# Optimization experiments

Measured on AMD Instinct MI355X. Metric: run time of the kernel, lower is better.

## Reference

```python
import jax, jax.numpy as jnp
import numpy as np

N_NODES = 50000
N_EDGES = 800000
NFEAT, NHID, NCLASS = 512, 128, 16


def _with_self_loops(edge_idx, n):
    loop = jnp.arange(n, dtype=edge_idx.dtype)
    src = jnp.concatenate([edge_idx[0], loop])  # [E+N]
    dst = jnp.concatenate([edge_idx[1], loop])
    return src, dst


def gcn_conv(x, src, dst, W, b, n):
    # GCNConv with add aggregation, self-loops, symmetric normalization.
    h = x @ W  # [N, out]
    ones = jnp.ones(src.shape[0], dtype=h.dtype)
    deg = jax.ops.segment_sum(ones, dst, num_segments=n)  # in-degree incl. self-loops
    dinv = jnp.where(deg > 0, jax.lax.rsqrt(deg), 0.0)
    norm = dinv[src] * dinv[dst]  # [E+N]
    msg = h[src] * norm[:, None]  # gather + scale
    out = jax.ops.segment_sum(msg, dst, num_segments=n)  # scatter-add
    return out + b


def setup_inputs() -> dict:
    key = jax.random.key(0)
    ks = jax.random.split(key, 8)
    x = jax.random.normal(ks[0], (N_NODES, NFEAT), dtype=jnp.float32)
    edge_idx = jax.random.randint(ks[1], (2, N_EDGES), 0, N_NODES, dtype=jnp.int64)
    s1 = 1.0 / np.sqrt(NFEAT)
    s2 = 1.0 / np.sqrt(NHID)
    W1 = jax.random.uniform(ks[2], (NFEAT, NHID), jnp.float32, -s1, s1)
    b1 = jnp.zeros((NHID,), jnp.float32)
    W2 = jax.random.uniform(ks[3], (NHID, NHID), jnp.float32, -s2, s2)
    b2 = jnp.zeros((NHID,), jnp.float32)
    Wc = jax.random.uniform(ks[4], (NHID, NCLASS), jnp.float32, -s2, s2)
    bc = jax.random.uniform(ks[5], (NCLASS,), jnp.float32, -s2, s2)
    return {"x": x, "edge_idx": edge_idx, "W1": W1, "b1": b1, "W2": W2, "b2": b2, "Wc": Wc, "bc": bc}


def reference(x, edge_idx, W1, b1, W2, b2, Wc, bc):
    n = x.shape[0]
    src, dst = _with_self_loops(edge_idx, n)
    h = gcn_conv(x, src, dst, W1, b1, n)
    h = jax.nn.relu(h)  # dropout is identity in eval mode
    h = gcn_conv(h, src, dst, W2, b2, n)
    h = jax.nn.relu(h)
    logits = h @ Wc + bc
    return jax.nn.log_softmax(logits, axis=1)
```

## Files before the change

kernel.cpp:

```cpp
#include <hip/hip_runtime.h>
#include <math.h>

#define NFEAT 512
#define NHID  128
#define NCLASS 16
#define SCAN_BS 512
#define AGG_BLOCKS 1024
#define NSTREAMS 16384

typedef __attribute__((ext_vector_type(8))) short short8;
typedef __attribute__((ext_vector_type(4))) float f32x4;

static __device__ __forceinline__ ushort f2b(float f) {
    union { float f; uint u; } v; v.f = f;
    uint r = v.u + 0x7FFFu + ((v.u >> 16) & 1u);
    return (ushort)(r >> 16);
}
static __device__ __forceinline__ float b2f_lo(uint bits) {
    union { uint u; float f; } v; v.u = bits << 16; return v.f;
}
static __device__ __forceinline__ float b2f_hi(uint bits) {
    union { uint u; float f; } v; v.u = bits & 0xffff0000u; return v.f;
}


__global__ void k_init_tcast(const float* __restrict__ W1, const float* __restrict__ W2,
                             ushort* __restrict__ W1T, ushort* __restrict__ W2T,
                             int* __restrict__ deg, int n) {
    int idx = blockIdx.x * 256 + threadIdx.x;
    if (idx < n) deg[idx] = 1;
    if (idx < NFEAT * 128) {
        int k = idx >> 7, c = idx & 127;
        W1T[(size_t)c * NFEAT + k] = f2b(W1[idx]);
    } else {
        int j = idx - NFEAT * 128;
        if (j < NHID * 128) {
            int k = j >> 7, c = j & 127;
            W2T[(size_t)c * NHID + k] = f2b(W2[j]);
        }
    }
}

__global__ void k_count(const int* __restrict__ dst, int e, int* __restrict__ deg,
                        int* __restrict__ ticket) {
    int i = blockIdx.x * blockDim.x + threadIdx.x;
    if (i < e) ticket[i] = atomicAdd(&deg[dst[i]], 1);
}

__global__ void k_scan1(const int* __restrict__ deg, float* __restrict__ dinv,
                        int* __restrict__ offs, int* __restrict__ bsum, int n) {
    __shared__ int s[SCAN_BS];
    int t = threadIdx.x;
    int i = blockIdx.x * SCAN_BS + t;
    int d = (i < n) ? deg[i] : 0;
    if (i < n) dinv[i] = rsqrtf((float)d);
    s[t] = d;
    for (int off = 1; off < SCAN_BS; off <<= 1) {
        __syncthreads();
        int x = (t >= off) ? s[t - off] : 0;
        __syncthreads();
        s[t] += x;
    }
    __syncthreads();
    if (i < n) offs[i] = s[t] - d;
    if (t == SCAN_BS - 1) bsum[blockIdx.x] = s[t];
}

__global__ void k_fill_edges(const int* __restrict__ src, const int* __restrict__ dst, int e,
                             const int* __restrict__ offs, const int* __restrict__ bsum,
                             const int* __restrict__ ticket, uint* __restrict__ colp32,
                             int* __restrict__ rankgs, int n, int S, int nbch) {
    __shared__ int incl[128];
    int tid = threadIdx.x;
    if (tid < 64) {
        int carry = 0;
        for (int base = 0; base < nbch; base += 64) {
            int j = base + tid;
            int v = (j < nbch) ? bsum[j] : 0;
            for (int off = 1; off < 64; off <<= 1) {
                int x = __shfl_up(v, off);
                if (tid >= off) v += x;
            }
            if (j < nbch) incl[j] = carry + v;
            carry += __shfl(v, 63);
        }
    }
    __syncthreads();

    auto absoff = [&](int v) -> int {
        if (v >= n) return S;
        int c = v >> 9;
        return offs[v] + (c ? incl[c - 1] : 0);
    };

    int i = blockIdx.x * blockDim.x + tid;
    if (i < e) {
        colp32[absoff(dst[i]) + ticket[i] - 1] = (uint)src[i];
    }
    if (i < n) {
        colp32[absoff(i + 1) - 1] = (uint)i | ((uint)(i + 1) << 16);
    }
    if (i < NSTREAMS) {
        int len = (S + NSTREAMS - 1) / NSTREAMS;
        int target = i * len;
        int lo = 0, hi = n;
        while (lo < hi) {
            int mid = (lo + hi) >> 1;
            if (absoff(mid) < target) lo = mid + 1; else hi = mid;
        }
        rankgs[i] = absoff(lo);
        if (i == 0) rankgs[NSTREAMS] = S;
    }
    if (i == 0) {
#pragma unroll
        for (int k = 0; k < 8; k++) colp32[S + k] = 0;
    }
}


template<int A_F32>
__global__ __launch_bounds__(256) void k_gemm(const void* __restrict__ Aptr,
                                              const ushort* __restrict__ WT,
                                              const float* __restrict__ rowscale,
                                              ushort* __restrict__ Hs, int M, int K) {
    __shared__ ushort As[64][40];
    __shared__ ushort Bs[128][40];

    const int tid = threadIdx.x;
    const int wc = tid >> 6, lane = tid & 63;
    const int lr = lane & 15, lk = (lane >> 4) * 8;
    const int rowbase = blockIdx.x * 64;

    f32x4 acc[4][2];
#pragma unroll
    for (int i = 0; i < 4; i++)
#pragma unroll
        for (int j = 0; j < 2; j++) acc[i][j] = (f32x4)0.f;

    const int sr = tid >> 2;
    const int sh = (tid & 3) * 8;

    for (int k0 = 0; k0 < K; k0 += 32) {
        {
            int gr = rowbase + sr;
            ushort tmp[8];
            if (A_F32) {
                const float* A = (const float*)Aptr;
                if (gr < M) {
                    const float* p = A + (size_t)gr * K + k0 + sh;
#pragma unroll
                    for (int q = 0; q < 2; q++) {
                        float4 v = *(const float4*)(p + q * 4);
                        tmp[q * 4 + 0] = f2b(v.x); tmp[q * 4 + 1] = f2b(v.y);
                        tmp[q * 4 + 2] = f2b(v.z); tmp[q * 4 + 3] = f2b(v.w);
                    }
                } else {
#pragma unroll
                    for (int q = 0; q < 8; q++) tmp[q] = 0;
                }
            } else {
                const ushort* A = (const ushort*)Aptr;
                if (gr < M) {
                    *(short8*)&tmp[0] = *(const short8*)(A + (size_t)gr * K + k0 + sh);
                } else {
#pragma unroll
                    for (int q = 0; q < 8; q++) tmp[q] = 0;
                }
            }
            *(short8*)&As[sr][sh] = *(short8*)&tmp[0];
        }
        {
#pragma unroll
            for (int t = 0; t < 2; t++) {
                int c = tid + t * 256;
                int row = c >> 2, q = c & 3;
                short8 v = *(const short8*)(WT + (size_t)row * K + k0 + q * 8);
                *(short8*)&Bs[row][q * 8] = v;
            }
        }
        __syncthreads();

        short8 af[4], bfv[2];
#pragma unroll
        for (int i = 0; i < 4; i++) af[i] = *(const short8*)&As[i * 16 + lr][lk];
#pragma unroll
        for (int j = 0; j < 2; j++) bfv[j] = *(const short8*)&Bs[wc * 32 + j * 16 + lr][lk];
#pragma unroll
        for (int i = 0; i < 4; i++)
#pragma unroll
            for (int j = 0; j < 2; j++)
                acc[i][j] = __builtin_amdgcn_mfma_f32_16x16x32_bf16(af[i], bfv[j], acc[i][j], 0, 0, 0);
        __syncthreads();
    }

#pragma unroll
    for (int i = 0; i < 4; i++) {
#pragma unroll
        for (int r = 0; r < 4; r++) {
            int row = rowbase + i * 16 + (lane >> 4) * 4 + r;
            if (row < M) {
                float sc = rowscale[row];
#pragma unroll
                for (int j = 0; j < 2; j++) {
                    int f = j * 16 + lr;
                    Hs[((size_t)wc * M + row) * 32 + f] = f2b(acc[i][j][r] * sc);
                }
            }
        }
    }
}


__global__ __launch_bounds__(256) void k_aggs(const ushort* __restrict__ hs,
                                              const uint* __restrict__ colp32,
                                              const int* __restrict__ rankgs,
                                              const float* __restrict__ dinv,
                                              const float* __restrict__ bias,
                                              ushort* __restrict__ outp, int n) {
    const int b = blockIdx.x;
    const int s = b & 3;
    const int wid = threadIdx.x >> 6, lane = threadIdx.x & 63;
    const int st16 = lane >> 2, q = lane & 3;
    const int stream = (((b >> 2) << 2) + wid) * 16 + st16;
    int g = rankgs[stream];
    int se = rankgs[stream + 1];
    bool alive = g < se;
    if (!alive) g = 0;

    const ushort* hsl = hs + (size_t)s * n * 32;
    const float4 bv0 = *(const float4*)(bias + s * 32 + q * 8);
    const float4 bv1 = *(const float4*)(bias + s * 32 + q * 8 + 4);

    const uint* cp = colp32 + g;
    uint cw0 = cp[0], cw1 = cp[1], cw2 = cp[2], cw3 = cp[3], cw4 = cp[4];
    uint4 pk0 = *(const uint4*)(hsl + (size_t)(cw0 & 0xffffu) * 32 + q * 8);
    uint4 pk1 = *(const uint4*)(hsl + (size_t)(cw1 & 0xffffu) * 32 + q * 8);
    uint4 pk2 = *(const uint4*)(hsl + (size_t)(cw2 & 0xffffu) * 32 + q * 8);
    uint4 pk3 = *(const uint4*)(hsl + (size_t)(cw3 & 0xffffu) * 32 + q * 8);
    float fdv0 = (cw0 >> 16) ? dinv[(cw0 >> 16) - 1] : 0.f;
    float fdv1 = (cw1 >> 16) ? dinv[(cw1 >> 16) - 1] : 0.f;
    float fdv2 = (cw2 >> 16) ? dinv[(cw2 >> 16) - 1] : 0.f;
    float fdv3 = (cw3 >> 16) ? dinv[(cw3 >> 16) - 1] : 0.f;
    float a0 = 0.f, a1 = 0.f, a2 = 0.f, a3 = 0.f;
    float a4 = 0.f, a5 = 0.f, a6 = 0.f, a7 = 0.f;

    while (__any(alive)) {
        if (alive) {
            uint cw5 = cp[5];
            uint4 pk4 = *(const uint4*)(hsl + (size_t)(cw4 & 0xffffu) * 32 + q * 8);
            float fdv4 = (cw4 >> 16) ? dinv[(cw4 >> 16) - 1] : 0.f;

            a0 += b2f_lo(pk0.x); a1 += b2f_hi(pk0.x);
            a2 += b2f_lo(pk0.y); a3 += b2f_hi(pk0.y);
            a4 += b2f_lo(pk0.z); a5 += b2f_hi(pk0.z);
            a6 += b2f_lo(pk0.w); a7 += b2f_hi(pk0.w);

            if (cw0 >> 16) {
                int v = (int)(cw0 >> 16) - 1;
                float r0 = fmaxf(fmaf(a0, fdv0, bv0.x), 0.f);
                float r1 = fmaxf(fmaf(a1, fdv0, bv0.y), 0.f);
                float r2 = fmaxf(fmaf(a2, fdv0, bv0.z), 0.f);
                float r3 = fmaxf(fmaf(a3, fdv0, bv0.w), 0.f);
                float r4 = fmaxf(fmaf(a4, fdv0, bv1.x), 0.f);
                float r5 = fmaxf(fmaf(a5, fdv0, bv1.y), 0.f);
                float r6 = fmaxf(fmaf(a6, fdv0, bv1.z), 0.f);
                float r7 = fmaxf(fmaf(a7, fdv0, bv1.w), 0.f);
                uint4 u;
                u.x = (uint)f2b(r0) | ((uint)f2b(r1) << 16);
                u.y = (uint)f2b(r2) | ((uint)f2b(r3) << 16);
                u.z = (uint)f2b(r4) | ((uint)f2b(r5) << 16);
                u.w = (uint)f2b(r6) | ((uint)f2b(r7) << 16);
                *(uint4*)(outp + (size_t)v * 128 + s * 32 + q * 8) = u;
                a0 = a1 = a2 = a3 = a4 = a5 = a6 = a7 = 0.f;
                if (g + 1 >= se) alive = false;
            }
            g++; cp++;
            cw0 = cw1; cw1 = cw2; cw2 = cw3; cw3 = cw4; cw4 = cw5;
            pk0 = pk1; pk1 = pk2; pk2 = pk3; pk3 = pk4;
            fdv0 = fdv1; fdv1 = fdv2; fdv2 = fdv3; fdv3 = fdv4;
        }
    }
}


__global__ __launch_bounds__(256) void k_classify(const ushort* __restrict__ h,
                                                  const float* __restrict__ Wc,
                                                  const float* __restrict__ bc,
                                                  float* __restrict__ out, int n) {
    __shared__ float Ws[128 * 16];
    int tid = threadIdx.x;
#pragma unroll
    for (int t = 0; t < 8; t++) Ws[tid + 256 * t] = Wc[tid + 256 * t];
    __syncthreads();

    int wid = tid >> 6, lane = tid & 63;
    int v = blockIdx.x * 4 + wid;
    if (v >= n) return;

    int j = lane & 15, c = lane >> 4;
    const ushort* hv = h + (size_t)v * 128 + c * 32;
    float acc = 0.f;
#pragma unroll
    for (int t = 0; t < 16; t++) {
        uint pk = *(const uint*)(hv + t * 2);
        acc = fmaf(b2f_lo(pk), Ws[(c * 32 + t * 2 + 0) * 16 + j], acc);
        acc = fmaf(b2f_hi(pk), Ws[(c * 32 + t * 2 + 1) * 16 + j], acc);
    }
    acc += __shfl_xor(acc, 16);
    acc += __shfl_xor(acc, 32);
    acc += bc[j];

    float m = acc;
#pragma unroll
    for (int o = 8; o >= 1; o >>= 1) m = fmaxf(m, __shfl_xor(m, o));
    float sum = expf(acc - m);
#pragma unroll
    for (int o = 8; o >= 1; o >>= 1) sum += __shfl_xor(sum, o);
    if (lane < 16) out[(size_t)v * 16 + j] = acc - m - logf(sum);
}


extern "C" void kernel_launch(void* const* d_in, const int* in_sizes, int n_in,
                              void* d_out, int out_size, void* d_ws, size_t ws_size,
                              hipStream_t stream) {
    const float* x  = (const float*)d_in[0];
    const int* eidx = (const int*)d_in[1];
    const float* W1 = (const float*)d_in[2];
    const float* b1 = (const float*)d_in[3];
    const float* W2 = (const float*)d_in[4];
    const float* b2 = (const float*)d_in[5];
    const float* Wc = (const float*)d_in[6];
    const float* bc = (const float*)d_in[7];
    float* out = (float*)d_out;

    const int N = in_sizes[0] / NFEAT;
    const int E = in_sizes[1] / 2;
    const int S = E + N;
    const int* src = eidx;
    const int* dst = eidx + E;

    char* p = (char*)d_ws;
    auto alloc = [&](size_t bytes) { char* r = p; p += (bytes + 255) & ~(size_t)255; return r; };
    int*    deg    = (int*)   alloc((size_t)N * 4);
    float*  dinv   = (float*) alloc((size_t)N * 4);
    int*    eoffs  = (int*)   alloc((size_t)(N + 1) * 4);
    int*    ticket = (int*)   alloc((size_t)E * 4);
    uint*   colp32 = (uint*)  alloc(((size_t)S + 16) * 4);
    int*    rankgs = (int*)   alloc((size_t)(NSTREAMS + 1) * 4);
    int*    bsum   = (int*)   alloc((size_t)256 * 4);
    ushort* W1T    = (ushort*)alloc((size_t)128 * NFEAT * 2);
    ushort* W2T    = (ushort*)alloc((size_t)128 * NHID * 2);
    ushort* hs     = (ushort*)alloc((size_t)N * NHID * 2);
    ushort* g1     = (ushort*)alloc((size_t)N * NHID * 2);
    ushort* g2     = (ushort*)alloc((size_t)N * NHID * 2);

    const int nb = (N + SCAN_BS - 1) / SCAN_BS;

    k_init_tcast<<<((NFEAT + NHID) * 128 + 255) / 256, 256, 0, stream>>>(W1, W2, W1T, W2T, deg, N);
    k_count<<<(E + 255) / 256, 256, 0, stream>>>(dst, E, deg, ticket);
    k_scan1<<<nb, SCAN_BS, 0, stream>>>(deg, dinv, eoffs, bsum, N);
    k_fill_edges<<<(E + 255) / 256, 256, 0, stream>>>(src, dst, E, eoffs, bsum, ticket,
                                                      colp32, rankgs, N, S, nb);

    const int gblocks = (N + 63) / 64;
    k_gemm<1><<<gblocks, 256, 0, stream>>>(x, W1T, dinv, hs, N, NFEAT);
    k_aggs<<<AGG_BLOCKS, 256, 0, stream>>>(hs, colp32, rankgs, dinv, b1, g1, N);
    k_gemm<0><<<gblocks, 256, 0, stream>>>(g1, W2T, dinv, hs, N, NHID);
    k_aggs<<<AGG_BLOCKS, 256, 0, stream>>>(hs, colp32, rankgs, dinv, b2, g2, N);
    k_classify<<<(N + 3) / 4, 256, 0, stream>>>(g2, Wc, bc, out, N);
}
```

Before: 228.8 us.

## Merge prep kernels, precompute per-edge dinv, double aggregation streams

Merges weight transpose/cast and degree counting into one kernel, with deg zeroed by memset and the self-loop added during the scan. Precomputes a per-entry dinv array next to the CSR column words, so the aggregation loop streams it sequentially instead of doing dependent gathers into dinv. Doubles the aggregation stream count and block count and adds an occupancy hint to launch_bounds. The cost is an extra S-sized float buffer and more segment-boundary overhead from the shorter streams.

Result: slower. 291.4 us (+27.4%).

```diff
diff --git a/kernel.cpp b/kernel.cpp
--- a/kernel.cpp
+++ b/kernel.cpp
@@ -5,8 +5,8 @@
 #define NHID  128
 #define NCLASS 16
 #define SCAN_BS 512
-#define AGG_BLOCKS 1024
-#define NSTREAMS 16384
+#define AGG_BLOCKS 2048
+#define NSTREAMS 32768
 
 typedef __attribute__((ext_vector_type(8))) short short8;
 typedef __attribute__((ext_vector_type(4))) float f32x4;
@@ -24,26 +24,21 @@
 }
 
 
-__global__ void k_init_tcast(const float* __restrict__ W1, const float* __restrict__ W2,
-                             ushort* __restrict__ W1T, ushort* __restrict__ W2T,
-                             int* __restrict__ deg, int n) {
-    int idx = blockIdx.x * 256 + threadIdx.x;
-    if (idx < n) deg[idx] = 1;
-    if (idx < NFEAT * 128) {
-        int k = idx >> 7, c = idx & 127;
-        W1T[(size_t)c * NFEAT + k] = f2b(W1[idx]);
-    } else {
-        int j = idx - NFEAT * 128;
-        if (j < NHID * 128) {
+__global__ void k_prep(const float* __restrict__ W1, const float* __restrict__ W2,
+                       ushort* __restrict__ W1T, ushort* __restrict__ W2T,
+                       const int* __restrict__ dst, int e,
+                       int* __restrict__ deg, int* __restrict__ ticket) {
+    int i = blockIdx.x * blockDim.x + threadIdx.x;
+    if (i < (NFEAT + NHID) * 128) {
+        if (i < NFEAT * 128) {
+            int k = i >> 7, c = i & 127;
+            W1T[(size_t)c * NFEAT + k] = f2b(W1[i]);
+        } else {
+            int j = i - NFEAT * 128;
             int k = j >> 7, c = j & 127;
             W2T[(size_t)c * NHID + k] = f2b(W2[j]);
         }
     }
-}
-
-__global__ void k_count(const int* __restrict__ dst, int e, int* __restrict__ deg,
-                        int* __restrict__ ticket) {
-    int i = blockIdx.x * blockDim.x + threadIdx.x;
     if (i < e) ticket[i] = atomicAdd(&deg[dst[i]], 1);
 }
 
@@ -52,7 +47,7 @@
     __shared__ int s[SCAN_BS];
     int t = threadIdx.x;
     int i = blockIdx.x * SCAN_BS + t;
-    int d = (i < n) ? deg[i] : 0;
+    int d = (i < n) ? (deg[i] + 1) : 0;
     if (i < n) dinv[i] = rsqrtf((float)d);
     s[t] = d;
     for (int off = 1; off < SCAN_BS; off <<= 1) {
@@ -69,7 +64,8 @@
 __global__ void k_fill_edges(const int* __restrict__ src, const int* __restrict__ dst, int e,
                              const int* __restrict__ offs, const int* __restrict__ bsum,
                              const int* __restrict__ ticket, uint* __restrict__ colp32,
-                             int* __restrict__ rankgs, int n, int S, int nbch) {
+                             float* __restrict__ fdvp, int* __restrict__ rankgs,
+                             int n, int S, int nbch) {
     __shared__ int incl[128];
     int tid = threadIdx.x;
     if (tid < 64) {
@@ -95,10 +91,12 @@
 
     int i = blockIdx.x * blockDim.x + tid;
     if (i < e) {
-        colp32[absoff(dst[i]) + ticket[i] - 1] = (uint)src[i];
+        colp32[absoff(dst[i]) + ticket[i]] = (uint)src[i];
     }
     if (i < n) {
-        colp32[absoff(i + 1) - 1] = (uint)i | ((uint)(i + 1) << 16);
+        int o0 = absoff(i), o1 = absoff(i + 1);
+        colp32[o1 - 1] = (uint)i | ((uint)(i + 1) << 16);
+        fdvp[o1 - 1] = rsqrtf((float)(o1 - o0));
     }
     if (i < NSTREAMS) {
         int len = (S + NSTREAMS - 1) / NSTREAMS;
@@ -211,12 +209,12 @@
 }
 
 
-__global__ __launch_bounds__(256) void k_aggs(const ushort* __restrict__ hs,
-                                              const uint* __restrict__ colp32,
-                                              const int* __restrict__ rankgs,
-                                              const float* __restrict__ dinv,
-                                              const float* __restrict__ bias,
-                                              ushort* __restrict__ outp, int n) {
+__global__ __launch_bounds__(256, 8) void k_aggs(const ushort* __restrict__ hs,
+                                                 const uint* __restrict__ colp32,
+                                                 const float* __restrict__ fdvp,
+                                                 const int* __restrict__ rankgs,
+                                                 const float* __restrict__ bias,
+                                                 ushort* __restrict__ outp, int n) {
     const int b = blockIdx.x;
     const int s = b & 3;
     const int wid = threadIdx.x >> 6, lane = threadIdx.x & 63;
@@ -232,23 +230,21 @@
     const float4 bv1 = *(const float4*)(bias + s * 32 + q * 8 + 4);
 
     const uint* cp = colp32 + g;
+    const float* fp = fdvp + g;
     uint cw0 = cp[0], cw1 = cp[1], cw2 = cp[2], cw3 = cp[3], cw4 = cp[4];
+    float fv0 = fp[0], fv1 = fp[1], fv2 = fp[2], fv3 = fp[3], fv4 = fp[4];
     uint4 pk0 = *(const uint4*)(hsl + (size_t)(cw0 & 0xffffu) * 32 + q * 8);
     uint4 pk1 = *(const uint4*)(hsl + (size_t)(cw1 & 0xffffu) * 32 + q * 8);
     uint4 pk2 = *(const uint4*)(hsl + (size_t)(cw2 & 0xffffu) * 32 + q * 8);
     uint4 pk3 = *(const uint4*)(hsl + (size_t)(cw3 & 0xffffu) * 32 + q * 8);
-    float fdv0 = (cw0 >> 16) ? dinv[(cw0 >> 16) - 1] : 0.f;
-    float fdv1 = (cw1 >> 16) ? dinv[(cw1 >> 16) - 1] : 0.f;
-    float fdv2 = (cw2 >> 16) ? dinv[(cw2 >> 16) - 1] : 0.f;
-    float fdv3 = (cw3 >> 16) ? dinv[(cw3 >> 16) - 1] : 0.f;
     float a0 = 0.f, a1 = 0.f, a2 = 0.f, a3 = 0.f;
     float a4 = 0.f, a5 = 0.f, a6 = 0.f, a7 = 0.f;
 
     while (__any(alive)) {
         if (alive) {
             uint cw5 = cp[5];
+            float fv5 = fp[5];
             uint4 pk4 = *(const uint4*)(hsl + (size_t)(cw4 & 0xffffu) * 32 + q * 8);
-            float fdv4 = (cw4 >> 16) ? dinv[(cw4 >> 16) - 1] : 0.f;
 
             a0 += b2f_lo(pk0.x); a1 += b2f_hi(pk0.x);
             a2 += b2f_lo(pk0.y); a3 += b2f_hi(pk0.y);
@@ -257,14 +253,14 @@
 
             if (cw0 >> 16) {
                 int v = (int)(cw0 >> 16) - 1;
-                float r0 = fmaxf(fmaf(a0, fdv0, bv0.x), 0.f);
-                float r1 = fmaxf(fmaf(a1, fdv0, bv0.y), 0.f);
-                float r2 = fmaxf(fmaf(a2, fdv0, bv0.z), 0.f);
-                float r3 = fmaxf(fmaf(a3, fdv0, bv0.w), 0.f);
-                float r4 = fmaxf(fmaf(a4, fdv0, bv1.x), 0.f);
-                float r5 = fmaxf(fmaf(a5, fdv0, bv1.y), 0.f);
-                float r6 = fmaxf(fmaf(a6, fdv0, bv1.z), 0.f);
-                float r7 = fmaxf(fmaf(a7, fdv0, bv1.w), 0.f);
+                float r0 = fmaxf(fmaf(a0, fv0, bv0.x), 0.f);
+                float r1 = fmaxf(fmaf(a1, fv0, bv0.y), 0.f);
+                float r2 = fmaxf(fmaf(a2, fv0, bv0.z), 0.f);
+                float r3 = fmaxf(fmaf(a3, fv0, bv0.w), 0.f);
+                float r4 = fmaxf(fmaf(a4, fv0, bv1.x), 0.f);
+                float r5 = fmaxf(fmaf(a5, fv0, bv1.y), 0.f);
+                float r6 = fmaxf(fmaf(a6, fv0, bv1.z), 0.f);
+                float r7 = fmaxf(fmaf(a7, fv0, bv1.w), 0.f);
                 uint4 u;
                 u.x = (uint)f2b(r0) | ((uint)f2b(r1) << 16);
                 u.y = (uint)f2b(r2) | ((uint)f2b(r3) << 16);
@@ -274,10 +270,10 @@
                 a0 = a1 = a2 = a3 = a4 = a5 = a6 = a7 = 0.f;
                 if (g + 1 >= se) alive = false;
             }
-            g++; cp++;
+            g++; cp++; fp++;
             cw0 = cw1; cw1 = cw2; cw2 = cw3; cw3 = cw4; cw4 = cw5;
+            fv0 = fv1; fv1 = fv2; fv2 = fv3; fv3 = fv4; fv4 = fv5;
             pk0 = pk1; pk1 = pk2; pk2 = pk3; pk3 = pk4;
-            fdv0 = fdv1; fdv1 = fdv2; fdv2 = fdv3; fdv3 = fdv4;
         }
     }
 }
@@ -346,6 +342,7 @@
     int*    eoffs  = (int*)   alloc((size_t)(N + 1) * 4);
     int*    ticket = (int*)   alloc((size_t)E * 4);
     uint*   colp32 = (uint*)  alloc(((size_t)S + 16) * 4);
+    float*  fdvp   = (float*) alloc(((size_t)S + 16) * 4);
     int*    rankgs = (int*)   alloc((size_t)(NSTREAMS + 1) * 4);
     int*    bsum   = (int*)   alloc((size_t)256 * 4);
     ushort* W1T    = (ushort*)alloc((size_t)128 * NFEAT * 2);
@@ -356,16 +353,16 @@
 
     const int nb = (N + SCAN_BS - 1) / SCAN_BS;
 
-    k_init_tcast<<<((NFEAT + NHID) * 128 + 255) / 256, 256, 0, stream>>>(W1, W2, W1T, W2T, deg, N);
-    k_count<<<(E + 255) / 256, 256, 0, stream>>>(dst, E, deg, ticket);
+    hipMemsetAsync(deg, 0, (size_t)N * 4, stream);
+    k_prep<<<(E + 255) / 256, 256, 0, stream>>>(W1, W2, W1T, W2T, dst, E, deg, ticket);
     k_scan1<<<nb, SCAN_BS, 0, stream>>>(deg, dinv, eoffs, bsum, N);
     k_fill_edges<<<(E + 255) / 256, 256, 0, stream>>>(src, dst, E, eoffs, bsum, ticket,
-                                                      colp32, rankgs, N, S, nb);
+                                                      colp32, fdvp, rankgs, N, S, nb);
 
     const int gblocks = (N + 63) / 64;
     k_gemm<1><<<gblocks, 256, 0, stream>>>(x, W1T, dinv, hs, N, NFEAT);
-    k_aggs<<<AGG_BLOCKS, 256, 0, stream>>>(hs, colp32, rankgs, dinv, b1, g1, N);
+    k_aggs<<<AGG_BLOCKS, 256, 0, stream>>>(hs, colp32, fdvp, rankgs, b1, g1, N);
     k_gemm<0><<<gblocks, 256, 0, stream>>>(g1, W2T, dinv, hs, N, NHID);
-    k_aggs<<<AGG_BLOCKS, 256, 0, stream>>>(hs, colp32, rankgs, dinv, b2, g2, N);
+    k_aggs<<<AGG_BLOCKS, 256, 0, stream>>>(hs, colp32, fdvp, rankgs, b2, g2, N);
     k_classify<<<(N + 3) / 4, 256, 0, stream>>>(g2, Wc, bc, out, N);
 }
```
